# Kernel tuning notes

Measured on AMD Instinct MI355X. Metric: run time of the kernel, lower is better.

Reference implementation:

```python
import jax, jax.numpy as jnp
import numpy as np
from jax import lax

B, N, C_PTS = 16, 4096, 64
NPOINT, RADIUS, NSAMPLE = 1024, 0.2, 32
MLP = [64, 64, 128]


def setup_inputs() -> dict:
    key = jax.random.key(0)
    ks = jax.random.split(key, 8)
    inp = {
        "xyz": jax.random.uniform(ks[0], (B, N, 3), jnp.float32),
        "points": jax.random.normal(ks[1], (B, N, C_PTS), jnp.float32),
    }
    cin = C_PTS + 3  # use_xyz=True concatenates centered xyz
    for i, cout in enumerate(MLP):
        inp[f"W{i}"] = jax.random.normal(ks[2 + 2 * i], (cin, cout), jnp.float32) / np.sqrt(cin).astype(np.float32)
        inp[f"b{i}"] = jnp.zeros((cout,), jnp.float32)
        cin = cout
    return inp


def _fps(xyz, npoint):
    # Farthest point sampling (sequential) -> (B, npoint) int32 indices.
    b, n, _ = xyz.shape

    def body(carry, _):
        mind, far = carry  # mind: (B,N) running min sq-dist, far: (B,) current pick
        cen = jnp.take_along_axis(xyz, far[:, None, None], axis=1)  # (B,1,3)
        d = jnp.sum((xyz - cen) ** 2, -1)  # (B,N)
        mind = jnp.minimum(mind, d)
        nxt = jnp.argmax(mind, -1).astype(jnp.int32)
        return (mind, nxt), far

    init = (jnp.full((b, n), 1e10, jnp.float32), jnp.zeros((b,), jnp.int32))
    _, idx = lax.scan(body, init, None, length=npoint)
    return jnp.transpose(idx)  # (B, npoint)


def _ball_query(radius, nsample, xyz, new_xyz):
    # First `nsample` point indices (in original order) within `radius` of each
    # center; short groups padded with the first found index (TF op semantics).
    n = xyz.shape[1]
    d2 = jnp.sum((new_xyz[:, :, None, :] - xyz[:, None, :, :]) ** 2, -1)  # (B,S,N)
    keyv = jnp.where(d2 <= radius * radius, jnp.arange(n, dtype=jnp.int32), n)
    idx = jnp.sort(keyv, axis=-1)[:, :, :nsample]  # smallest indices first
    first = idx[:, :, :1]
    idx = jnp.where(idx == n, first, idx)
    return jnp.minimum(idx, n - 1)


def _group(t, idx):
    # t: (B,N,C), idx: (B,S,K) -> (B,S,K,C)
    return jax.vmap(lambda tb, ib: tb[ib])(t, idx)


def reference(xyz, points, W0, b0, W1, b1, W2, b2):
    fps_idx = _fps(xyz, NPOINT)  # (B,S)
    new_xyz = jnp.take_along_axis(xyz, fps_idx[..., None], axis=1)  # (B,S,3)
    idx = _ball_query(RADIUS, NSAMPLE, xyz, new_xyz)  # (B,S,K)
    grouped_xyz = _group(xyz, idx) - new_xyz[:, :, None, :]  # (B,S,K,3) centered
    grouped_pts = _group(points, idx)  # (B,S,K,C)
    new_points = jnp.concatenate([grouped_xyz, grouped_pts], -1)  # (B,S,K,3+C)
    for W, b in ((W0, b0), (W1, b1), (W2, b2)):  # shared MLP = 1x1 conv + relu
        new_points = jax.nn.relu(jnp.einsum('bskc,cd->bskd', new_points, W) + b)
    new_points = jnp.max(new_points, axis=2)  # max-pool over neighbors -> (B,S,128)
    return new_xyz, new_points, idx
```

## Files before the change

kernel.cpp:

```cpp
#include <hip/hip_runtime.h>

#define NB      16
#define NPTS    4096
#define NPOINT  1024
#define NSAMPLE 32

template <int C>
__device__ __forceinline__ int dppi(int v) {
  return __builtin_amdgcn_update_dpp(0, v, C, 0xf, 0xf, true);
}

template <int C>
__device__ __forceinline__ unsigned long long dppmax_u64(unsigned long long k) {
  int lo = dppi<C>((int)(unsigned)k);
  int hi = dppi<C>((int)(k >> 32));
  unsigned long long o = ((unsigned long long)(unsigned)hi << 32) | (unsigned)lo;
  return o > k ? o : k;
}

__device__ __forceinline__ unsigned long long swzmax16_u64(unsigned long long k) {
  int lo = __builtin_amdgcn_ds_swizzle((int)(unsigned)k, 0x401F);
  int hi = __builtin_amdgcn_ds_swizzle((int)(k >> 32), 0x401F);
  unsigned long long o = ((unsigned long long)(unsigned)hi << 32) | (unsigned)lo;
  return o > k ? o : k;
}

__device__ __forceinline__ unsigned long long bpermmax32_u64(unsigned long long k, int addr) {
  int lo = __builtin_amdgcn_ds_bpermute(addr, (int)(unsigned)k);
  int hi = __builtin_amdgcn_ds_bpermute(addr, (int)(k >> 32));
  unsigned long long o = ((unsigned long long)(unsigned)hi << 32) | (unsigned)lo;
  return o > k ? o : k;
}

__global__ __launch_bounds__(512) void fps_kernel(const float* __restrict__ xyz,
                                                  float* __restrict__ out_xyz) {
  __shared__ float lx[NPTS], ly[NPTS], lz[NPTS];
  __shared__ unsigned long long part[2][8];
  const int b = blockIdx.x, t = threadIdx.x;
  const int lane = t & 63;
  const float* g = xyz + (size_t)b * NPTS * 3;
  for (int j = t; j < NPTS; j += 512) {
    lx[j] = g[3 * j]; ly[j] = g[3 * j + 1]; lz[j] = g[3 * j + 2];
  }
  __syncthreads();
  float px[8], py[8], pz[8], mind[8];
#pragma unroll
  for (int i = 0; i < 8; ++i) {
    const int j = t + 512 * i;
    px[i] = lx[j]; py[i] = ly[j]; pz[i] = lz[j];
    mind[i] = 1e10f;
  }
  const int baddr = ((lane ^ 32) & 63) << 2;
  float cx = lx[0], cy = ly[0], cz = lz[0];
  float* ob = out_xyz + (size_t)b * NPOINT * 3;
  for (int it = 0; it < NPOINT; ++it) {
    if (t == 0) { ob[3 * it] = cx; ob[3 * it + 1] = cy; ob[3 * it + 2] = cz; }
    float vmax = -1.0f;
    unsigned aj = 0;
#pragma unroll
    for (int i = 0; i < 8; ++i) {
      const float dx = __fsub_rn(px[i], cx);
      const float dy = __fsub_rn(py[i], cy);
      const float dz = __fsub_rn(pz[i], cz);
      const float d2 = __fadd_rn(__fadd_rn(__fmul_rn(dx, dx), __fmul_rn(dy, dy)),
                                 __fmul_rn(dz, dz));
      const float m = fminf(mind[i], d2);
      mind[i] = m;
      if (m > vmax) { vmax = m; aj = (unsigned)(t + 512 * i); }
    }
    unsigned long long key =
        ((unsigned long long)__float_as_uint(vmax) << 32) | (unsigned)(~aj);
    key = dppmax_u64<0xB1>(key);
    key = dppmax_u64<0x4E>(key);
    key = dppmax_u64<0x141>(key);
    key = dppmax_u64<0x140>(key);
    key = swzmax16_u64(key);
    key = bpermmax32_u64(key, baddr);
    const int buf = it & 1;
    if (lane == 0) part[buf][t >> 6] = key;
    __syncthreads();
    unsigned long long rk = part[buf][lane & 7];
    rk = dppmax_u64<0xB1>(rk);
    rk = dppmax_u64<0x4E>(rk);
    rk = dppmax_u64<0x141>(rk);
    const unsigned idx = ~(unsigned)rk;
    cx = lx[idx]; cy = ly[idx]; cz = lz[idx];
  }
}

__global__ __launch_bounds__(256) void ballq_kernel(const float* __restrict__ xyz,
                                                    const float* __restrict__ new_xyz,
                                                    int* __restrict__ ballidx,
                                                    float* __restrict__ out_idx) {
  __shared__ int sidx[4][NSAMPLE];
  const int wv = threadIdx.x >> 6, lane = threadIdx.x & 63;
  const int q = blockIdx.x * 4 + wv;
  const int b = q >> 10;
  const float* g = xyz + (size_t)b * NPTS * 3;
  const float nx = new_xyz[(size_t)q * 3];
  const float ny = new_xyz[(size_t)q * 3 + 1];
  const float nz = new_xyz[(size_t)q * 3 + 2];
  const float r2 = (float)(0.2 * 0.2);
  int cnt = 0;
  for (int base = 0; base < NPTS; base += 64) {
    const int j = base + lane;
    const float dx = __fsub_rn(g[3 * j], nx);
    const float dy = __fsub_rn(g[3 * j + 1], ny);
    const float dz = __fsub_rn(g[3 * j + 2], nz);
    const float d2 = __fadd_rn(__fadd_rn(__fmul_rn(dx, dx), __fmul_rn(dy, dy)),
                               __fmul_rn(dz, dz));
    const bool hit = d2 <= r2;
    const unsigned long long m = __ballot(hit);
    const int pos = cnt + __popcll(m & ((1ull << lane) - 1ull));
    if (hit && pos < NSAMPLE) sidx[wv][pos] = j;
    cnt += __popcll(m);
    if (cnt >= NSAMPLE) break;
  }
  __syncthreads();
  const int capped = cnt < NSAMPLE ? cnt : NSAMPLE;
  if (lane < NSAMPLE) {
    const int v = sidx[wv][lane < capped ? lane : 0];
    ballidx[(size_t)q * NSAMPLE + lane] = v;
    out_idx[(size_t)q * NSAMPLE + lane] = (float)v;
  }
}

__global__ __launch_bounds__(256) void p1_kernel(const float* __restrict__ pts,
                                                 const float* __restrict__ W0,
                                                 float* __restrict__ P1) {
  __shared__ float sw[4096];
  const int t = threadIdx.x;
  {
    const float4* w4 = (const float4*)(W0 + 192);
    float4* s4 = (float4*)sw;
#pragma unroll
    for (int m = 0; m < 4; ++m) s4[t + 256 * m] = w4[t + 256 * m];
  }
  __syncthreads();
  const size_t r = (size_t)blockIdx.x * 256 + t;
  const float* prow = pts + r * 64;
  float acc[64];
#pragma unroll
  for (int d = 0; d < 64; ++d) acc[d] = 0.0f;
#pragma unroll
  for (int cq = 0; cq < 16; ++cq) {
    const float4 p4 = *(const float4*)(prow + cq * 4);
    const float pv[4] = {p4.x, p4.y, p4.z, p4.w};
#pragma unroll
    for (int u = 0; u < 4; ++u) {
      const int c = cq * 4 + u;
#pragma unroll
      for (int d4 = 0; d4 < 16; ++d4) {
        const float4 w = *(const float4*)(&sw[c * 64 + d4 * 4]);
        acc[d4 * 4 + 0] = fmaf(pv[u], w.x, acc[d4 * 4 + 0]);
        acc[d4 * 4 + 1] = fmaf(pv[u], w.y, acc[d4 * 4 + 1]);
        acc[d4 * 4 + 2] = fmaf(pv[u], w.z, acc[d4 * 4 + 2]);
        acc[d4 * 4 + 3] = fmaf(pv[u], w.w, acc[d4 * 4 + 3]);
      }
    }
  }
  float* o = P1 + r * 64;
#pragma unroll
  for (int d4 = 0; d4 < 16; ++d4)
    *(float4*)(o + d4 * 4) =
        make_float4(acc[d4 * 4], acc[d4 * 4 + 1], acc[d4 * 4 + 2], acc[d4 * 4 + 3]);
}

__global__ __launch_bounds__(256) void mlp_kernel(
    const float* __restrict__ xyz, const float* __restrict__ new_xyz,
    const int* __restrict__ ballidx, const float* __restrict__ P1,
    const float* __restrict__ W0, const float* __restrict__ b0,
    const float* __restrict__ W1, const float* __restrict__ b1,
    const float* __restrict__ W2, const float* __restrict__ b2,
    float* __restrict__ out_np) {
  const int t = threadIdx.x;
  const int item = blockIdx.x * 256 + t;
  const int k = item & 31;
  const int q = item >> 5;
  const int b = q >> 10;
  const int idx = ballidx[(size_t)q * 32 + k];
  const float nx = new_xyz[(size_t)q * 3];
  const float ny = new_xyz[(size_t)q * 3 + 1];
  const float nz = new_xyz[(size_t)q * 3 + 2];
  const float* p = xyz + ((size_t)b * NPTS + idx) * 3;
  const float dx = p[0] - nx, dy = p[1] - ny, dz = p[2] - nz;

  float h1[64];
  const float* p1r = P1 + ((size_t)b * NPTS + idx) * 64;
#pragma unroll
  for (int d4 = 0; d4 < 16; ++d4) {
    const float4 pv = *(const float4*)(p1r + d4 * 4);
    const float pe[4] = {pv.x, pv.y, pv.z, pv.w};
#pragma unroll
    for (int u = 0; u < 4; ++u) {
      const int d = d4 * 4 + u;
      const float v = pe[u] + dx * W0[d] + dy * W0[64 + d] + dz * W0[128 + d] + b0[d];
      h1[d] = fmaxf(v, 0.0f);
    }
  }

  float h2[64];
#pragma unroll
  for (int j4 = 0; j4 < 16; ++j4) {
    const float4 bb = *(const float4*)(&b1[j4 * 4]);
    h2[j4 * 4 + 0] = bb.x; h2[j4 * 4 + 1] = bb.y;
    h2[j4 * 4 + 2] = bb.z; h2[j4 * 4 + 3] = bb.w;
  }
#pragma unroll
  for (int c = 0; c < 64; ++c) {
    const float hc = h1[c];
#pragma unroll
    for (int j4 = 0; j4 < 16; ++j4) {
      const float4 w = *(const float4*)(&W1[c * 64 + j4 * 4]);
      h2[j4 * 4 + 0] = fmaf(hc, w.x, h2[j4 * 4 + 0]);
      h2[j4 * 4 + 1] = fmaf(hc, w.y, h2[j4 * 4 + 1]);
      h2[j4 * 4 + 2] = fmaf(hc, w.z, h2[j4 * 4 + 2]);
      h2[j4 * 4 + 3] = fmaf(hc, w.w, h2[j4 * 4 + 3]);
    }
  }
#pragma unroll
  for (int j = 0; j < 64; ++j) h2[j] = fmaxf(h2[j], 0.0f);

  float* outq = out_np + (size_t)q * 128;
  for (int jb = 0; jb < 4; ++jb) {
    float acc[32];
#pragma unroll
    for (int j8 = 0; j8 < 8; ++j8) {
      const float4 bb = *(const float4*)(&b2[jb * 32 + j8 * 4]);
      acc[j8 * 4 + 0] = bb.x; acc[j8 * 4 + 1] = bb.y;
      acc[j8 * 4 + 2] = bb.z; acc[j8 * 4 + 3] = bb.w;
    }
#pragma unroll
    for (int c = 0; c < 64; ++c) {
      const float hc = h2[c];
#pragma unroll
      for (int j8 = 0; j8 < 8; ++j8) {
        const float4 w = *(const float4*)(&W2[c * 128 + jb * 32 + j8 * 4]);
        acc[j8 * 4 + 0] = fmaf(hc, w.x, acc[j8 * 4 + 0]);
        acc[j8 * 4 + 1] = fmaf(hc, w.y, acc[j8 * 4 + 1]);
        acc[j8 * 4 + 2] = fmaf(hc, w.z, acc[j8 * 4 + 2]);
        acc[j8 * 4 + 3] = fmaf(hc, w.w, acc[j8 * 4 + 3]);
      }
    }
#pragma unroll
    for (int j = 0; j < 32; ++j) acc[j] = fmaxf(acc[j], 0.0f);
#pragma unroll
    for (int msk = 16; msk >= 1; msk >>= 1) {
#pragma unroll
      for (int j = 0; j < 32; ++j) acc[j] = fmaxf(acc[j], __shfl_xor(acc[j], msk, 64));
    }
    if (k == 0) {
#pragma unroll
      for (int j8 = 0; j8 < 8; ++j8)
        *(float4*)(outq + jb * 32 + j8 * 4) =
            make_float4(acc[j8 * 4 + 0], acc[j8 * 4 + 1], acc[j8 * 4 + 2], acc[j8 * 4 + 3]);
    }
  }
}

extern "C" void kernel_launch(void* const* d_in, const int* in_sizes, int n_in,
                              void* d_out, int out_size, void* d_ws, size_t ws_size,
                              hipStream_t stream) {
  const float* xyz = (const float*)d_in[0];
  const float* pts = (const float*)d_in[1];
  const float* W0  = (const float*)d_in[2];
  const float* b0  = (const float*)d_in[3];
  const float* W1  = (const float*)d_in[4];
  const float* b1  = (const float*)d_in[5];
  const float* W2  = (const float*)d_in[6];
  const float* b2  = (const float*)d_in[7];

  float* out      = (float*)d_out;
  float* out_xyz  = out;
  float* out_np   = out + 16 * 1024 * 3;
  float* out_idx  = out_np + 16 * 1024 * 128;

  int*   ballidx = (int*)d_ws;
  float* P1      = (float*)((char*)d_ws + (2u << 20));

  fps_kernel<<<NB, 512, 0, stream>>>(xyz, out_xyz);
  p1_kernel<<<256, 256, 0, stream>>>(pts, W0, P1);
  ballq_kernel<<<4096, 256, 0, stream>>>(xyz, out_xyz, ballidx, out_idx);
  mlp_kernel<<<2048, 256, 0, stream>>>(xyz, out_xyz, ballidx, P1,
                                       W0, b0, W1, b1, W2, b2, out_np);
}
```

Before: 1.005 ms.

## Pack FPS distance math into v_pk_f32 ops and shorten per-iteration argmax reduction

Rewrites the farthest-point-sampling inner loop so two points are handled per packed f32 instruction (v_pk_add/v_pk_mul) instead of scalar sub/mul/add. The per-thread argmax becomes a 64-bit key tree max over the 8 candidates. The cross-lane ds_bpermute step is dropped: each half-wave writes its partial to shared memory and the block reduction grows to 16 entries with one extra DPP step. Centroid output is buffered in LDS and written to global memory once at the end rather than every iteration. The packed asm is less flexible for the compiler's scheduling, and the fminf on each packed half stays scalar.

```diff
diff --git a/kernel.cpp b/kernel.cpp
--- a/kernel.cpp
+++ b/kernel.cpp
@@ -4,6 +4,22 @@
 #define NPTS    4096
 #define NPOINT  1024
 #define NSAMPLE 32
+
+typedef float v2f __attribute__((ext_vector_type(2)));
+
+__device__ __forceinline__ v2f pk_add(v2f a, v2f b) {
+  v2f d;
+  asm("v_pk_add_f32 %0, %1, %2" : "=v"(d) : "v"(a), "v"(b));
+  return d;
+}
+__device__ __forceinline__ v2f pk_mul(v2f a, v2f b) {
+  v2f d;
+  asm("v_pk_mul_f32 %0, %1, %2" : "=v"(d) : "v"(a), "v"(b));
+  return d;
+}
+__device__ __forceinline__ float fnegx(float x) {
+  return __int_as_float(__float_as_int(x) ^ 0x80000000);
+}
 
 template <int C>
 __device__ __forceinline__ int dppi(int v) {
@@ -25,67 +41,84 @@
   return o > k ? o : k;
 }
 
-__device__ __forceinline__ unsigned long long bpermmax32_u64(unsigned long long k, int addr) {
-  int lo = __builtin_amdgcn_ds_bpermute(addr, (int)(unsigned)k);
-  int hi = __builtin_amdgcn_ds_bpermute(addr, (int)(k >> 32));
-  unsigned long long o = ((unsigned long long)(unsigned)hi << 32) | (unsigned)lo;
-  return o > k ? o : k;
-}
-
 __global__ __launch_bounds__(512) void fps_kernel(const float* __restrict__ xyz,
                                                   float* __restrict__ out_xyz) {
   __shared__ float lx[NPTS], ly[NPTS], lz[NPTS];
-  __shared__ unsigned long long part[2][8];
+  __shared__ float scen[NPOINT * 3];
+  __shared__ unsigned long long part[2][16];
   const int b = blockIdx.x, t = threadIdx.x;
   const int lane = t & 63;
+  const int wid = t >> 6;
   const float* g = xyz + (size_t)b * NPTS * 3;
   for (int j = t; j < NPTS; j += 512) {
     lx[j] = g[3 * j]; ly[j] = g[3 * j + 1]; lz[j] = g[3 * j + 2];
   }
   __syncthreads();
-  float px[8], py[8], pz[8], mind[8];
-#pragma unroll
-  for (int i = 0; i < 8; ++i) {
-    const int j = t + 512 * i;
-    px[i] = lx[j]; py[i] = ly[j]; pz[i] = lz[j];
-    mind[i] = 1e10f;
-  }
-  const int baddr = ((lane ^ 32) & 63) << 2;
+  v2f px2[4], py2[4], pz2[4], mind2[4];
+  unsigned nlo[8];
+#pragma unroll
+  for (int p = 0; p < 4; ++p) {
+    const int j0 = t + 512 * (2 * p);
+    px2[p] = (v2f){lx[j0], lx[j0 + 512]};
+    py2[p] = (v2f){ly[j0], ly[j0 + 512]};
+    pz2[p] = (v2f){lz[j0], lz[j0 + 512]};
+    mind2[p] = (v2f){1e10f, 1e10f};
+    nlo[2 * p] = ~(unsigned)j0;
+    nlo[2 * p + 1] = ~(unsigned)(j0 + 512);
+  }
   float cx = lx[0], cy = ly[0], cz = lz[0];
-  float* ob = out_xyz + (size_t)b * NPOINT * 3;
   for (int it = 0; it < NPOINT; ++it) {
-    if (t == 0) { ob[3 * it] = cx; ob[3 * it + 1] = cy; ob[3 * it + 2] = cz; }
-    float vmax = -1.0f;
-    unsigned aj = 0;
-#pragma unroll
-    for (int i = 0; i < 8; ++i) {
-      const float dx = __fsub_rn(px[i], cx);
-      const float dy = __fsub_rn(py[i], cy);
-      const float dz = __fsub_rn(pz[i], cz);
-      const float d2 = __fadd_rn(__fadd_rn(__fmul_rn(dx, dx), __fmul_rn(dy, dy)),
-                                 __fmul_rn(dz, dz));
-      const float m = fminf(mind[i], d2);
-      mind[i] = m;
-      if (m > vmax) { vmax = m; aj = (unsigned)(t + 512 * i); }
-    }
-    unsigned long long key =
-        ((unsigned long long)__float_as_uint(vmax) << 32) | (unsigned)(~aj);
+    if (t == 0) {
+      scen[3 * it] = cx; scen[3 * it + 1] = cy; scen[3 * it + 2] = cz;
+    }
+    const float ncx = fnegx(cx), ncy = fnegx(cy), ncz = fnegx(cz);
+    const v2f ncxx = (v2f){ncx, ncx};
+    const v2f ncyy = (v2f){ncy, ncy};
+    const v2f nczz = (v2f){ncz, ncz};
+#pragma unroll
+    for (int p = 0; p < 4; ++p) {
+      const v2f dx = pk_add(px2[p], ncxx);
+      const v2f dy = pk_add(py2[p], ncyy);
+      const v2f dz = pk_add(pz2[p], nczz);
+      const v2f xx = pk_mul(dx, dx);
+      const v2f yy = pk_mul(dy, dy);
+      const v2f zz = pk_mul(dz, dz);
+      v2f s = pk_add(xx, yy);
+      s = pk_add(s, zz);
+      mind2[p].x = fminf(mind2[p].x, s.x);
+      mind2[p].y = fminf(mind2[p].y, s.y);
+    }
+    unsigned long long k[8];
+#pragma unroll
+    for (int p = 0; p < 4; ++p) {
+      k[2 * p] = ((unsigned long long)__float_as_uint(mind2[p].x) << 32) | nlo[2 * p];
+      k[2 * p + 1] =
+          ((unsigned long long)__float_as_uint(mind2[p].y) << 32) | nlo[2 * p + 1];
+    }
+#pragma unroll
+    for (int s = 4; s; s >>= 1)
+#pragma unroll
+      for (int i = 0; i < s; ++i) k[i] = k[i] > k[i + s] ? k[i] : k[i + s];
+    unsigned long long key = k[0];
     key = dppmax_u64<0xB1>(key);
     key = dppmax_u64<0x4E>(key);
     key = dppmax_u64<0x141>(key);
     key = dppmax_u64<0x140>(key);
     key = swzmax16_u64(key);
-    key = bpermmax32_u64(key, baddr);
     const int buf = it & 1;
-    if (lane == 0) part[buf][t >> 6] = key;
+    if ((lane & 31) == 0) part[buf][wid * 2 + (lane >> 5)] = key;
     __syncthreads();
-    unsigned long long rk = part[buf][lane & 7];
+    unsigned long long rk = part[buf][lane & 15];
     rk = dppmax_u64<0xB1>(rk);
     rk = dppmax_u64<0x4E>(rk);
     rk = dppmax_u64<0x141>(rk);
+    rk = dppmax_u64<0x140>(rk);
     const unsigned idx = ~(unsigned)rk;
     cx = lx[idx]; cy = ly[idx]; cz = lz[idx];
   }
+  __syncthreads();
+  float* ob = out_xyz + (size_t)b * NPOINT * 3;
+  for (int i = t; i < NPOINT * 3; i += 512) ob[i] = scen[i];
 }
 
 __global__ __launch_bounds__(256) void ballq_kernel(const float* __restrict__ xyz,
```

Result: faster. 953.4 us (-5.2%).
